# Kernel tuning notes

Hardware: AMD Instinct MI355X
Metric: run time of the kernel (lower is better)

The kernel has to match this reference:

```python
import jax, jax.numpy as jnp
import numpy as np
from jax import lax

HUMAN_CONF = 0.7
IOU_TH = 0.5


def setup_inputs() -> dict:
    key = jax.random.key(0)
    k1, k2 = jax.random.split(key)
    B, Q, C = 16, 2048, 2
    return {
        "human_logits": jax.random.normal(k1, (B, Q, C), dtype=jnp.float32),
        "pred_boxes": jax.random.uniform(k2, (B, Q, 4), dtype=jnp.float32),  # cxcywh in [0,1]
        "img_h": 800,
        "img_w": 1333,
    }


def box_cxcywh_to_xyxy(b):
    cx, cy, w, h = b[..., 0], b[..., 1], b[..., 2], b[..., 3]
    return jnp.stack([cx - 0.5 * w, cy - 0.5 * h, cx + 0.5 * w, cy + 0.5 * h], axis=-1)


def pairwise_iou(b):
    # b: [Q,4] xyxy -> iou: [Q,Q]
    area = jnp.clip(b[:, 2] - b[:, 0], 0) * jnp.clip(b[:, 3] - b[:, 1], 0)
    lt = jnp.maximum(b[:, None, :2], b[None, :, :2])
    rb = jnp.minimum(b[:, None, 2:], b[None, :, 2:])
    wh = jnp.clip(rb - lt, 0)
    inter = wh[..., 0] * wh[..., 1]
    union = area[:, None] + area[None, :] - inter
    return inter / jnp.maximum(union, 1e-9)


def nms_keep(boxes, scores, valid, iou_th):
    # Greedy NMS on one image with fixed shapes; returns keep mask [Q].
    Q = scores.shape[0]
    order = jnp.argsort(jnp.where(valid, -scores, jnp.inf))  # valid boxes first, score desc
    b = boxes[order]
    v = valid[order]
    iou = pairwise_iou(b)                       # [Q,Q]
    idx = jnp.arange(Q)
    sup_mat = (iou > iou_th) & (idx[None, :] > idx[:, None])  # i suppresses later j

    def step(supp, i):
        keep_i = v[i] & jnp.logical_not(supp[i])
        supp = supp | (keep_i & sup_mat[i])
        return supp, keep_i

    _, keep_sorted = lax.scan(step, jnp.zeros(Q, bool), idx)
    return jnp.zeros(Q, bool).at[order].set(keep_sorted)


def reference(human_logits, pred_boxes, img_h, img_w):
    prob = jax.nn.softmax(human_logits, axis=-1)          # [B,Q,C]
    scores = prob.max(axis=-1)                            # [B,Q]
    labels = prob.argmax(axis=-1)                         # [B,Q]
    boxes = box_cxcywh_to_xyxy(pred_boxes)                # [B,Q,4]
    scale = jnp.array([img_w, img_h, img_w, img_h], dtype=boxes.dtype)
    boxes = boxes * scale
    valid = (labels == 0) & (scores >= HUMAN_CONF)
    keep = jax.vmap(lambda b, s, v: nms_keep(b, s, v, IOU_TH))(boxes, scores, valid)
    scores_out = jnp.where(keep, scores, 0.0)
    boxes_out = jnp.where(keep[..., None], boxes, 0.0).astype(jnp.int32)
    return scores_out, boxes_out, keep
```

## Files before the change

kernel.cpp:

```cpp
#include <hip/hip_runtime.h>
#include <math.h>


#define QN    2048
#define NS    1024
#define MATW  17408
#define MAGIC 0x5ca1ab1eu

__device__ __forceinline__ int rb32(int wb) { return 64 * wb * (33 - wb); }

__device__ __forceinline__ unsigned long long shfl_xor_u64(unsigned long long x, int m) {
    int lo = __shfl_xor((int)(unsigned)(x & 0xffffffffull), m, 64);
    int hi = __shfl_xor((int)(unsigned)(x >> 32), m, 64);
    return ((unsigned long long)(unsigned)hi << 32) | (unsigned)lo;
}

__device__ __forceinline__ unsigned long long score_key(float2 l, int q, bool* valid_out) {
    float mx = fmaxf(l.x, l.y), mn = fminf(l.x, l.y);
    float e = expf(mn - mx);
    float score = 1.0f / (1.0f + e);
    bool valid = (l.x >= l.y) && (score >= 0.7f);
    *valid_out = valid;
    unsigned sbits = valid ? __float_as_uint(score) : 0u;
    return ((unsigned long long)(~sbits) << 32) | (unsigned)q;
}

__global__ __launch_bounds__(1024) void kfused(
    const float* __restrict__ logits, const float* __restrict__ pboxes,
    const int* __restrict__ img_h_p, const int* __restrict__ img_w_p,
    unsigned* __restrict__ wflag, unsigned* __restrict__ wmat,
    float* __restrict__ out, int B)
{
    __shared__ __align__(16) char smem[32904];
    unsigned long long* skey = (unsigned long long*)smem;
    float* sx1 = (float*)(smem + 8192);
    float* sy1 = (float*)(smem + 12288);
    float* sx2 = (float*)(smem + 16384);
    float* sy2 = (float*)(smem + 20480);
    float* sar = (float*)(smem + 24576);
    unsigned short* sidxl = (unsigned short*)(smem + 28672);
    unsigned char* keepq = (unsigned char*)(smem + 30720);
    unsigned* skm = (unsigned*)(smem + 32768);
    int* sMp = (int*)(smem + 32896);

    const int blk = blockIdx.x;
    const int b = blk % B, slice = blk / B;
    const int tid = threadIdx.x, lane = tid & 63, wave = tid >> 6;
    const float sw = (float)(*img_w_p), sh = (float)(*img_h_p);

    if (tid == 0) *sMp = 0;
    __syncthreads();

    const unsigned long long lmask_lt = (1ull << lane) - 1ull;
#pragma unroll
    for (int qq = 0; qq < 2; ++qq) {
        int q = tid + qq * 1024;
        float2 l = ((const float2*)logits)[b * QN + q];
        bool valid;
        unsigned long long key = score_key(l, q, &valid);
        unsigned long long mb = __ballot(valid);
        int base = 0;
        if (lane == 0 && mb) base = atomicAdd(sMp, __popcll(mb));
        base = __shfl(base, 0, 64);
        if (valid) {
            int slot = base + __popcll(mb & lmask_lt);
            if (slot < NS) skey[slot] = key;
        }
    }
    __syncthreads();
    const int M = *sMp;

    if (M <= NS) {
        unsigned long long v = (tid < M) ? skey[tid] : ~0ull;
        __syncthreads();
#pragma unroll
        for (int k = 2; k <= 64; k <<= 1) {
            bool dir = ((tid & k) == 0);
#pragma unroll
            for (int j = k >> 1; j > 0; j >>= 1) {
                unsigned long long o = shfl_xor_u64(v, j);
                bool takeMin = (dir == ((tid & j) == 0));
                v = ((v < o) == takeMin) ? v : o;
            }
        }
        for (int k = 128; k <= NS; k <<= 1) {
            bool dir = ((tid & k) == 0);
            for (int j = k >> 1; j >= 64; j >>= 1) {
                skey[tid] = v;
                __syncthreads();
                unsigned long long o = skey[tid ^ j];
                bool takeMin = (dir == ((tid & j) == 0));
                v = ((v < o) == takeMin) ? v : o;
                __syncthreads();
            }
#pragma unroll
            for (int j = 32; j > 0; j >>= 1) {
                unsigned long long o = shfl_xor_u64(v, j);
                bool takeMin = (dir == ((tid & j) == 0));
                v = ((v < o) == takeMin) ? v : o;
            }
        }
        int qi = (int)((unsigned)v & 0xffffu);
        const int NG = (M + 3) >> 2;

        if (slice != 0) {
            float x1 = 0.f, y1 = 0.f, x2 = 0.f, y2 = 0.f, ar = 0.f;
            if (tid < M) {
                float4 pb = ((const float4*)pboxes)[b * QN + qi];
                x1 = (pb.x - 0.5f * pb.z) * sw;
                y1 = (pb.y - 0.5f * pb.w) * sh;
                x2 = (pb.x + 0.5f * pb.z) * sw;
                y2 = (pb.y + 0.5f * pb.w) * sh;
                ar = fmaxf(x2 - x1, 0.f) * fmaxf(y2 - y1, 0.f);
            }
            sx1[tid] = x1; sy1[tid] = y1; sx2[tid] = x2; sy2[tid] = y2; sar[tid] = ar;
            __syncthreads();

            unsigned* mat = wmat + (long)b * MATW;
            const int W64 = (M + 63) >> 6;
            for (int gi = (slice - 1) * 16 + wave; gi < NG; gi += 112) {
                const int g = gi << 2;
                const int nr = min(4, M - g);
                const int wb = g >> 6;
                const int rl = 32 - 2 * wb;
                float ax1[4], ay1[4], ax2[4], ay2[4], aar[4];
                int rbase[4];
#pragma unroll
                for (int r = 0; r < 4; ++r) {
                    int i = g + min(r, nr - 1);
                    ax1[r] = sx1[i]; ay1[r] = sy1[i];
                    ax2[r] = sx2[i]; ay2[r] = sy2[i]; aar[r] = sar[i];
                    rbase[r] = rb32(wb) + ((g + r) & 63) * rl;
                }
                for (int w = wb; w < W64; ++w) {
                    int j = (w << 6) | lane;
                    float bx1 = sx1[j], by1 = sy1[j], bx2 = sx2[j], by2 = sy2[j], bar = sar[j];
#pragma unroll
                    for (int r = 0; r < 4; ++r) {
                        float ltx = fmaxf(ax1[r], bx1), lty = fmaxf(ay1[r], by1);
                        float rbx = fminf(ax2[r], bx2), rby = fminf(ay2[r], by2);
                        float wx = fmaxf(rbx - ltx, 0.f), wy = fmaxf(rby - lty, 0.f);
                        float inter = wx * wy;
                        float uni = aar[r] + bar - inter;
                        float iou = inter / fmaxf(uni, 1e-9f);
                        bool sup = (iou > 0.5f) && (j > g + r);
                        unsigned long long bal = __ballot(sup);
                        if (lane == 0 && r < nr)
                            __hip_atomic_store(
                                (unsigned long long*)(mat + rbase[r] + 2 * (w - wb)), bal,
                                __ATOMIC_RELAXED, __HIP_MEMORY_SCOPE_AGENT);
                    }
                }
            }
            __syncthreads();
            if (tid == 0)
                __hip_atomic_store(&wflag[b * 8 + slice], MAGIC,
                                   __ATOMIC_RELEASE, __HIP_MEMORY_SCOPE_AGENT);
            return;
        }

        sidxl[tid] = (unsigned short)qi;
        keepq[tid] = 0; keepq[tid + 1024] = 0;
        if (tid < 32) skm[tid] = 0;

        float2 l2a = ((const float2*)logits)[b * QN + tid];
        float2 l2b = ((const float2*)logits)[b * QN + tid + 1024];
        float4 p4a = ((const float4*)pboxes)[b * QN + tid];
        float4 p4b = ((const float4*)pboxes)[b * QN + tid + 1024];

        if (wave == 0) {
            const unsigned* fp = &wflag[b * 8 + 1 + lane];
            for (;;) {
                unsigned f = (lane < 7)
                    ? __hip_atomic_load(fp, __ATOMIC_RELAXED, __HIP_MEMORY_SCOPE_AGENT)
                    : MAGIC;
                if (__all(f == MAGIC)) break;
                __builtin_amdgcn_s_sleep(2);
            }
            (void)__hip_atomic_load(&wflag[b * 8 + 1], __ATOMIC_ACQUIRE,
                                    __HIP_MEMORY_SCOPE_AGENT);

            const unsigned* gm = wmat + (long)b * MATW;
            unsigned rem = 0;
            const int Ms = __builtin_amdgcn_readfirstlane(M);
            const int C = (Ms + 31) >> 5;
            unsigned rcur[32], rnxt[32];
            if (C > 0) {
                int Lc = min(tid, 31);
#pragma unroll
                for (int t = 0; t < 32; ++t) rcur[t] = gm[Lc + t * 32];
            }
            for (int c = 0; c < C; ++c) {
                if (c + 1 < C) {
                    int cn = c + 1, wbn = cn >> 1, rln = 32 - 2 * wbn;
                    int Lcn = min(max(tid, 2 * wbn), 31);
                    int rb0n = rb32(wbn) + ((cn & 1) << 5) * rln + (Lcn - 2 * wbn);
#pragma unroll
                    for (int t = 0; t < 32; ++t) rnxt[t] = gm[rb0n + t * rln];
                }
                unsigned rw = (unsigned)__builtin_amdgcn_readlane((int)rem, c);
                unsigned keepmask = 0;
                int lim = min(32, Ms - (c << 5));
#pragma unroll
                for (int t = 0; t < 32; ++t) {
                    if (t < lim && !((rw >> t) & 1u)) {
                        keepmask |= (1u << t);
                        rem |= rcur[t];
                        rw |= (unsigned)__builtin_amdgcn_readlane((int)rcur[t], c);
                    }
                }
                if (tid == 0) skm[c] = keepmask;
                if (c + 1 < C) {
#pragma unroll
                    for (int t = 0; t < 32; ++t) rcur[t] = rnxt[t];
                }
            }
        }
        __syncthreads();
        for (int s = tid; s < M; s += 1024)
            if ((skm[s >> 5] >> (s & 31)) & 1u) keepq[sidxl[s]] = 1;
        __syncthreads();

        const long BQ = (long)B * QN;
#pragma unroll
        for (int qq = 0; qq < 2; ++qq) {
            int q = tid + qq * 1024;
            int base = b * QN + q;
            float2 l = qq ? l2b : l2a;
            float4 pb = qq ? p4b : p4a;
            float e = expf(fminf(l.x, l.y) - fmaxf(l.x, l.y));
            float score = 1.0f / (1.0f + e);
            float x1 = (pb.x - 0.5f * pb.z) * sw, y1 = (pb.y - 0.5f * pb.w) * sh;
            float x2 = (pb.x + 0.5f * pb.z) * sw, y2 = (pb.y + 0.5f * pb.w) * sh;
            int kp = keepq[q];
            out[base] = kp ? score : 0.f;
            out[BQ * 5 + base] = kp ? 1.f : 0.f;
            float4 ob;
            ob.x = kp ? truncf(x1) : 0.f;
            ob.y = kp ? truncf(y1) : 0.f;
            ob.z = kp ? truncf(x2) : 0.f;
            ob.w = kp ? truncf(y2) : 0.f;
            ((float4*)(out + BQ))[base] = ob;
        }
    } else {
        if (slice != 0) return;
        unsigned long long* skeyF = (unsigned long long*)smem;
        unsigned char* ssupp = (unsigned char*)(smem + 16384);
        keepq[tid] = 0; keepq[tid + 1024] = 0;
        for (int q = tid; q < QN; q += 1024) {
            float2 l = ((const float2*)logits)[b * QN + q];
            bool valid;
            skeyF[q] = score_key(l, q, &valid);
        }
        __syncthreads();
        for (int k = 2; k <= QN; k <<= 1)
            for (int j = k >> 1; j > 0; j >>= 1) {
                int i = ((tid & ~(j - 1)) << 1) | (tid & (j - 1));
                int p = i | j;
                bool up = ((i & k) == 0);
                unsigned long long a = skeyF[i], c2 = skeyF[p];
                if ((a > c2) == up) { skeyF[i] = c2; skeyF[p] = a; }
                __syncthreads();
            }
        for (int s = tid; s < M; s += 1024) ssupp[s] = 0;
        __syncthreads();
        for (int i = 0; i < M; ++i) {
            __syncthreads();
            if (ssupp[i]) continue;
            int ia = (unsigned short)(unsigned)skeyF[i];
            float4 pa = ((const float4*)pboxes)[b * QN + ia];
            float ax1 = (pa.x - 0.5f * pa.z) * sw, ay1 = (pa.y - 0.5f * pa.w) * sh;
            float ax2 = (pa.x + 0.5f * pa.z) * sw, ay2 = (pa.y + 0.5f * pa.w) * sh;
            float areaA = fmaxf(ax2 - ax1, 0.f) * fmaxf(ay2 - ay1, 0.f);
            for (int jj = i + 1 + tid; jj < M; jj += 1024) {
                int jb = (unsigned short)(unsigned)skeyF[jj];
                float4 pq = ((const float4*)pboxes)[b * QN + jb];
                float bx1 = (pq.x - 0.5f * pq.z) * sw, by1 = (pq.y - 0.5f * pq.w) * sh;
                float bx2 = (pq.x + 0.5f * pq.z) * sw, by2 = (pq.y + 0.5f * pq.w) * sh;
                float ltx = fmaxf(ax1, bx1), lty = fmaxf(ay1, by1);
                float rbx = fminf(ax2, bx2), rby = fminf(ay2, by2);
                float wx = fmaxf(rbx - ltx, 0.f), wy = fmaxf(rby - lty, 0.f);
                float inter = wx * wy;
                float areaB = fmaxf(bx2 - bx1, 0.f) * fmaxf(by2 - by1, 0.f);
                float uni = areaA + areaB - inter;
                if (inter / fmaxf(uni, 1e-9f) > 0.5f) ssupp[jj] = 1;
            }
        }
        __syncthreads();
        for (int s = tid; s < M; s += 1024)
            if (!ssupp[s]) keepq[(unsigned short)(unsigned)skeyF[s]] = 1;
        __syncthreads();

        const long BQ = (long)B * QN;
#pragma unroll
        for (int qq = 0; qq < 2; ++qq) {
            int q = tid + qq * 1024;
            int base = b * QN + q;
            float2 l = ((const float2*)logits)[base];
            float e = expf(fminf(l.x, l.y) - fmaxf(l.x, l.y));
            float score = 1.0f / (1.0f + e);
            float4 pb = ((const float4*)pboxes)[base];
            float x1 = (pb.x - 0.5f * pb.z) * sw, y1 = (pb.y - 0.5f * pb.w) * sh;
            float x2 = (pb.x + 0.5f * pb.z) * sw, y2 = (pb.y + 0.5f * pb.w) * sh;
            int kp = keepq[q];
            out[base] = kp ? score : 0.f;
            out[BQ * 5 + base] = kp ? 1.f : 0.f;
            float4 ob;
            ob.x = kp ? truncf(x1) : 0.f;
            ob.y = kp ? truncf(y1) : 0.f;
            ob.z = kp ? truncf(x2) : 0.f;
            ob.w = kp ? truncf(y2) : 0.f;
            ((float4*)(out + BQ))[base] = ob;
        }
    }
}

extern "C" void kernel_launch(void* const* d_in, const int* in_sizes, int n_in,
                              void* d_out, int out_size, void* d_ws, size_t ws_size,
                              hipStream_t stream) {
    const float* logits = (const float*)d_in[0];
    const float* pboxes = (const float*)d_in[1];
    const int*   img_h  = (const int*)d_in[2];
    const int*   img_w  = (const int*)d_in[3];
    float* out = (float*)d_out;
    const int B = in_sizes[0] / (QN * 2);

    char* ws = (char*)d_ws;
    unsigned* wflag = (unsigned*)(ws + 0);
    unsigned* wmat  = (unsigned*)(ws + 1024);

    kfused<<<dim3(B * 8), dim3(1024), 0, stream>>>(logits, pboxes, img_h, img_w,
                                                   wflag, wmat, out, B);
}
```

Measured before the change: 103.4 us.

## Replace bitonic sort with rank-by-counting scatter for score ordering

Swaps the shared-memory and shuffle bitonic sort of up to 1024 score keys for a rank sort: each thread counts how many keys are smaller than its own and scatters its box data to that rank. This drops the many barrier-separated merge stages of the bitonic network. In exchange each thread does O(M) shared-memory reads, which are broadcast reads of the same address, and a few extra barriers are added to zero the arrays before the scatter.

Measured after the change: 108.8 us. +5.3%, slower.

```diff
diff --git a/kernel.cpp b/kernel.cpp
--- a/kernel.cpp
+++ b/kernel.cpp
@@ -8,12 +8,6 @@
 #define MAGIC 0x5ca1ab1eu
 
 __device__ __forceinline__ int rb32(int wb) { return 64 * wb * (33 - wb); }
-
-__device__ __forceinline__ unsigned long long shfl_xor_u64(unsigned long long x, int m) {
-    int lo = __shfl_xor((int)(unsigned)(x & 0xffffffffull), m, 64);
-    int hi = __shfl_xor((int)(unsigned)(x >> 32), m, 64);
-    return ((unsigned long long)(unsigned)hi << 32) | (unsigned)lo;
-}
 
 __device__ __forceinline__ unsigned long long score_key(float2 l, int q, bool* valid_out) {
     float mx = fmaxf(l.x, l.y), mn = fminf(l.x, l.y);
@@ -71,49 +65,33 @@
     const int M = *sMp;
 
     if (M <= NS) {
-        unsigned long long v = (tid < M) ? skey[tid] : ~0ull;
-        __syncthreads();
-#pragma unroll
-        for (int k = 2; k <= 64; k <<= 1) {
-            bool dir = ((tid & k) == 0);
-#pragma unroll
-            for (int j = k >> 1; j > 0; j >>= 1) {
-                unsigned long long o = shfl_xor_u64(v, j);
-                bool takeMin = (dir == ((tid & j) == 0));
-                v = ((v < o) == takeMin) ? v : o;
-            }
-        }
-        for (int k = 128; k <= NS; k <<= 1) {
-            bool dir = ((tid & k) == 0);
-            for (int j = k >> 1; j >= 64; j >>= 1) {
-                skey[tid] = v;
-                __syncthreads();
-                unsigned long long o = skey[tid ^ j];
-                bool takeMin = (dir == ((tid & j) == 0));
-                v = ((v < o) == takeMin) ? v : o;
-                __syncthreads();
-            }
-#pragma unroll
-            for (int j = 32; j > 0; j >>= 1) {
-                unsigned long long o = shfl_xor_u64(v, j);
-                bool takeMin = (dir == ((tid & j) == 0));
-                v = ((v < o) == takeMin) ? v : o;
-            }
-        }
-        int qi = (int)((unsigned)v & 0xffffu);
+        int rnk = -1;
+        unsigned long long my = 0;
+        if (tid < M) {
+            my = skey[tid];
+            int r = 0, j = 0;
+            for (; j + 4 <= M; j += 4)
+                r += (int)(skey[j] < my) + (int)(skey[j + 1] < my)
+                   + (int)(skey[j + 2] < my) + (int)(skey[j + 3] < my);
+            for (; j < M; ++j) r += (int)(skey[j] < my);
+            rnk = r;
+        }
+        const int qi = (int)((unsigned)my & 0xffffu);
         const int NG = (M + 3) >> 2;
 
         if (slice != 0) {
-            float x1 = 0.f, y1 = 0.f, x2 = 0.f, y2 = 0.f, ar = 0.f;
+            sx1[tid] = 0.f; sy1[tid] = 0.f; sx2[tid] = 0.f;
+            sy2[tid] = 0.f; sar[tid] = 0.f;
+            __syncthreads();
             if (tid < M) {
                 float4 pb = ((const float4*)pboxes)[b * QN + qi];
-                x1 = (pb.x - 0.5f * pb.z) * sw;
-                y1 = (pb.y - 0.5f * pb.w) * sh;
-                x2 = (pb.x + 0.5f * pb.z) * sw;
-                y2 = (pb.y + 0.5f * pb.w) * sh;
-                ar = fmaxf(x2 - x1, 0.f) * fmaxf(y2 - y1, 0.f);
-            }
-            sx1[tid] = x1; sy1[tid] = y1; sx2[tid] = x2; sy2[tid] = y2; sar[tid] = ar;
+                float x1 = (pb.x - 0.5f * pb.z) * sw;
+                float y1 = (pb.y - 0.5f * pb.w) * sh;
+                float x2 = (pb.x + 0.5f * pb.z) * sw;
+                float y2 = (pb.y + 0.5f * pb.w) * sh;
+                sx1[rnk] = x1; sy1[rnk] = y1; sx2[rnk] = x2; sy2[rnk] = y2;
+                sar[rnk] = fmaxf(x2 - x1, 0.f) * fmaxf(y2 - y1, 0.f);
+            }
             __syncthreads();
 
             unsigned* mat = wmat + (long)b * MATW;
@@ -159,14 +137,17 @@
             return;
         }
 
-        sidxl[tid] = (unsigned short)qi;
+        sidxl[tid] = 0;
         keepq[tid] = 0; keepq[tid + 1024] = 0;
         if (tid < 32) skm[tid] = 0;
+        __syncthreads();
+        if (tid < M) sidxl[rnk] = (unsigned short)qi;
 
         float2 l2a = ((const float2*)logits)[b * QN + tid];
         float2 l2b = ((const float2*)logits)[b * QN + tid + 1024];
         float4 p4a = ((const float4*)pboxes)[b * QN + tid];
         float4 p4b = ((const float4*)pboxes)[b * QN + tid + 1024];
+        __syncthreads();
 
         if (wave == 0) {
             const unsigned* fp = &wflag[b * 8 + 1 + lane];
```
